# Kernel optimization log

Hardware: AMD Instinct MI355X
Metric: run time of the kernel (lower is better)

Reference implementation:

```python
import jax, jax.numpy as jnp
import numpy as np

TOPOLOGY = [-1, 0, 0, 0, 1, 2, 3, 4, 5, 6, 7, 8, 9, 9, 9, 12, 13, 14, 16, 17, 18, 19, 20, 21]
JOINT_WEIGHTS = np.ones(24, dtype=np.float32)
B1 = 1.0
B2 = 1.0


def quaternion_to_matrix(q):
    # pytorch3d convention: real part first (w, x, y, z)
    w, x, y, z = q[..., 0], q[..., 1], q[..., 2], q[..., 3]
    two_s = 2.0 / jnp.sum(q * q, axis=-1)
    o = jnp.stack([
        1 - two_s * (y * y + z * z), two_s * (x * y - z * w), two_s * (x * z + y * w),
        two_s * (x * y + z * w), 1 - two_s * (x * x + z * z), two_s * (y * z - x * w),
        two_s * (x * z - y * w), two_s * (y * z + x * w), 1 - two_s * (x * x + y * y),
    ], axis=-1)
    return o.reshape(q.shape[:-1] + (3, 3))


def fk(topology, X_m, X_t):
    # X_m: (bs, T, J*4+3), X_t: (bs, J, 3)
    J = len(topology)
    quat = X_m[..., :-3].reshape(X_m.shape[:-1] + (J, 4))
    local_rot = quaternion_to_matrix(quat)          # (bs, T, J, 3, 3)
    grots = [None] * J
    gtrs = [None] * J
    grots[0] = local_rot[..., 0, :, :]
    gtrs[0] = X_m[..., -3:]                          # root translation
    for i in range(1, J):
        pi = topology[i]
        grots[i] = jnp.matmul(grots[pi], local_rot[..., i, :, :])
        gtrs[i] = jnp.einsum('btij,bj->bti', grots[pi], X_t[:, i]) + gtrs[pi]
    return jnp.stack(grots, axis=-3), jnp.stack(gtrs, axis=-2)


def split_raw_motion(raw_motion):
    position = raw_motion[..., -3:]
    rotation = raw_motion[..., :-3]
    rotation = rotation.reshape(rotation.shape[:-1] + (-1, 4))
    norm = jnp.linalg.norm(rotation, axis=-1, keepdims=True)
    rotation = rotation / jnp.maximum(norm, 1e-12)
    return rotation, position


def weighted_mse(w, a, b):
    # w: (J,), a/b: (bs, T, J, C) -> per-joint weighted mean squared error
    return jnp.mean(w[None, None, :, None] * (a - b) ** 2)


def setup_inputs() -> dict:
    key = jax.random.key(0)
    k1, k2, k3, k4 = jax.random.split(key, 4)
    bs, T, J = 64, 2048, 24
    return {
        'Y_m': jax.random.normal(k1, (bs, T, J * 4 + 3), dtype=jnp.float32),
        'X_m': jax.random.normal(k2, (bs, T, J * 4 + 3), dtype=jnp.float32),
        'Y_t': jax.random.normal(k3, (bs, J, 3), dtype=jnp.float32),
        'X_t': jax.random.normal(k4, (bs, J, 3), dtype=jnp.float32),
    }


def reference(Y_m, X_m, Y_t, X_t):
    w = jnp.asarray(JOINT_WEIGHTS)
    rot_x, pos_x = split_raw_motion(X_m)
    rot_y, pos_y = split_raw_motion(Y_m)
    grot_y, gtr_y = fk(TOPOLOGY, Y_m, Y_t)
    grot_x, gtr_x = fk(TOPOLOGY, X_m, X_t)
    loss_rot = B1 * weighted_mse(w, rot_y, rot_x)
    loss_fk = B2 * (2.5 * weighted_mse(w, gtr_y, gtr_x)
                    + jnp.mean((pos_y - pos_x) ** 2))
    return loss_rot + loss_fk
```

## Files before the change

### kernel.cpp

```cpp
#include <hip/hip_runtime.h>

#define BS 64
#define TT 2048
#define NJ 24
#define ROWF 99
#define TROWS 128
#define BLOCK 128
#define NROWS (BS * TT)

__device__ __forceinline__ void quat2mat(float w, float x, float y, float z, float* R) {
  float s = 2.0f / (w*w + x*x + y*y + z*z);
  float xx = s*x*x, yy = s*y*y, zz = s*z*z;
  float xy = s*x*y, xz = s*x*z, yz = s*y*z;
  float xw = s*x*w, yw = s*y*w, zw = s*z*w;
  R[0] = 1.0f - (yy+zz); R[1] = xy - zw;        R[2] = xz + yw;
  R[3] = xy + zw;        R[4] = 1.0f - (xx+zz); R[5] = yz - xw;
  R[6] = xz - yw;        R[7] = yz + xw;        R[8] = 1.0f - (xx+yy);
}

__device__ __forceinline__ void mm3(const float* A, const float* B, float* C) {
#pragma unroll
  for (int r = 0; r < 3; ++r) {
#pragma unroll
    for (int c = 0; c < 3; ++c) {
      C[3*r+c] = fmaf(A[3*r], B[c], fmaf(A[3*r+1], B[3+c], A[3*r+2]*B[6+c]));
    }
  }
}

template<int PHASE>
__device__ __forceinline__ void fk_chain(const float* __restrict__ rowp,
                                         const float* __restrict__ tvec,
                                         float* __restrict__ gtr, float& gacc) {
  float G0[9], Ga[9], Gb[9], G9[9];
  float T0[3], Ta[3], Tb[3], T9[3];

  quat2mat(rowp[0], rowp[1], rowp[2], rowp[3], G0);
  T0[0] = rowp[96]; T0[1] = rowp[97]; T0[2] = rowp[98];
  if (PHASE == 0) { gtr[0] = T0[0]; gtr[1] = T0[1]; gtr[2] = T0[2]; }
  else { float d0 = T0[0]-gtr[0], d1 = T0[1]-gtr[1], d2 = T0[2]-gtr[2];
         gacc += d0*d0 + d1*d1 + d2*d2; }

#define STEP(c, Gp, Tp, Go, To) do { \
    float R[9]; quat2mat(rowp[4*(c)], rowp[4*(c)+1], rowp[4*(c)+2], rowp[4*(c)+3], R); \
    mm3(Gp, R, Go); \
    To[0] = fmaf(Gp[0], tvec[3*(c)], fmaf(Gp[1], tvec[3*(c)+1], fmaf(Gp[2], tvec[3*(c)+2], Tp[0]))); \
    To[1] = fmaf(Gp[3], tvec[3*(c)], fmaf(Gp[4], tvec[3*(c)+1], fmaf(Gp[5], tvec[3*(c)+2], Tp[1]))); \
    To[2] = fmaf(Gp[6], tvec[3*(c)], fmaf(Gp[7], tvec[3*(c)+1], fmaf(Gp[8], tvec[3*(c)+2], Tp[2]))); \
    if (PHASE == 0) { gtr[3*(c)] = To[0]; gtr[3*(c)+1] = To[1]; gtr[3*(c)+2] = To[2]; } \
    else { float d0 = To[0]-gtr[3*(c)], d1 = To[1]-gtr[3*(c)+1], d2 = To[2]-gtr[3*(c)+2]; \
           gacc += d0*d0 + d1*d1 + d2*d2; } \
  } while (0)

  STEP(1,  G0, T0, Ga, Ta); STEP(4,  Ga, Ta, Gb, Tb); STEP(7,  Gb, Tb, Ga, Ta); STEP(10, Ga, Ta, Gb, Tb);
  STEP(2,  G0, T0, Ga, Ta); STEP(5,  Ga, Ta, Gb, Tb); STEP(8,  Gb, Tb, Ga, Ta); STEP(11, Ga, Ta, Gb, Tb);
  STEP(3,  G0, T0, Ga, Ta); STEP(6,  Ga, Ta, Gb, Tb); STEP(9,  Gb, Tb, G9, T9);
  STEP(12, G9, T9, Ga, Ta); STEP(15, Ga, Ta, Gb, Tb);
  STEP(13, G9, T9, Ga, Ta); STEP(16, Ga, Ta, Gb, Tb); STEP(18, Gb, Tb, Ga, Ta); STEP(20, Ga, Ta, Gb, Tb); STEP(22, Gb, Tb, Ga, Ta);
  STEP(14, G9, T9, Ga, Ta); STEP(17, Ga, Ta, Gb, Tb); STEP(19, Gb, Tb, Ga, Ta); STEP(21, Ga, Ta, Gb, Tb); STEP(23, Gb, Tb, Ga, Ta);
#undef STEP
}

__global__ __launch_bounds__(BLOCK, 2) void motion_loss_kernel(
    const float* __restrict__ Ym, const float* __restrict__ Xm,
    const float* __restrict__ Yt, const float* __restrict__ Xt,
    float* __restrict__ out) {
  __shared__ __align__(16) float tile[TROWS * ROWF];
  __shared__ float tX[NJ * 3], tY[NJ * 3];

  const int tid = threadIdx.x;
  const int blk = blockIdx.x;
  const size_t row0 = (size_t)blk * TROWS;
  const int b = blk / (TT / TROWS);

  if (tid < NJ * 3) {
    tX[tid] = Xt[(size_t)b * NJ * 3 + tid];
    tY[tid] = Yt[(size_t)b * NJ * 3 + tid];
  }

  {
    const float4* g4 = (const float4*)(Xm + row0 * ROWF);
    float4* l4 = (float4*)tile;
    for (int k = tid; k < TROWS * ROWF / 4; k += BLOCK) l4[k] = g4[k];
  }
  __syncthreads();

  float gtrX[NJ * 3];
  float gacc = 0.0f, dummy = 0.0f;
  const float* rowp = tile + tid * ROWF;
  fk_chain<0>(rowp, tX, gtrX, dummy);
  __syncthreads();

  float rot_acc = 0.0f, pos_acc = 0.0f;
  const float* __restrict__ Yg = Ym + row0 * ROWF;
#pragma unroll 4
  for (int k = 0; k < NJ; ++k) {
    int q = tid + k * BLOCK;
    int r = q / NJ;
    int j = q - r * NJ;
    int off = r * ROWF + 4 * j;
    float y0 = Yg[off], y1 = Yg[off+1], y2 = Yg[off+2], y3 = Yg[off+3];
    float x0 = tile[off], x1 = tile[off+1], x2 = tile[off+2], x3 = tile[off+3];
    float ny = fmaxf(sqrtf(y0*y0 + y1*y1 + y2*y2 + y3*y3), 1e-12f);
    float nx = fmaxf(sqrtf(x0*x0 + x1*x1 + x2*x2 + x3*x3), 1e-12f);
    float iy = 1.0f / ny, ix = 1.0f / nx;
    float d0 = y0*iy - x0*ix, d1 = y1*iy - x1*ix;
    float d2 = y2*iy - x2*ix, d3 = y3*iy - x3*ix;
    rot_acc += d0*d0 + d1*d1 + d2*d2 + d3*d3;
    tile[off] = y0; tile[off+1] = y1; tile[off+2] = y2; tile[off+3] = y3;
  }
#pragma unroll
  for (int k = 0; k < 3; ++k) {
    int e = tid + k * BLOCK;
    int r = e / 3;
    int c = e - r * 3;
    int off = r * ROWF + 96 + c;
    float y = Yg[off], x = tile[off];
    float d = y - x;
    pos_acc += d * d;
    tile[off] = y;
  }
  __syncthreads();

  fk_chain<1>(rowp, tY, gtrX, gacc);

  const float c_rot = 1.0f / ((float)NROWS * NJ * 4);
  const float c_gtr = 2.5f / ((float)NROWS * NJ * 3);
  const float c_pos = 1.0f / ((float)NROWS * 3);
  float contrib = c_rot * rot_acc + c_gtr * gacc + c_pos * pos_acc;
#pragma unroll
  for (int o = 32; o > 0; o >>= 1) contrib += __shfl_down(contrib, o, 64);
  if ((tid & 63) == 0) atomicAdd(out, contrib);
}

extern "C" void kernel_launch(void* const* d_in, const int* in_sizes, int n_in,
                              void* d_out, int out_size, void* d_ws, size_t ws_size,
                              hipStream_t stream) {
  const float* Ym = (const float*)d_in[0];
  const float* Xm = (const float*)d_in[1];
  const float* Yt = (const float*)d_in[2];
  const float* Xt = (const float*)d_in[3];
  float* out = (float*)d_out;
  hipMemsetAsync(out, 0, sizeof(float), stream);
  motion_loss_kernel<<<NROWS / TROWS, BLOCK, 0, stream>>>(Ym, Xm, Yt, Xt, out);
}
```

Before: 167.9 us.

## Pair X and Y rows across adjacent lanes, exchange diffs via shuffles, drop LDS tiling

Each row is now handled by two adjacent threads, one running forward kinematics on X and the other on Y. Differences are exchanged with __shfl_xor instead of staging the X tile in LDS and keeping 72 per-thread registers of X translations. The joint tree is re-scheduled with four rotating register buffers, and leaf joints skip their unused matrix product. Global loads become uncoalesced strided unaligned float4 reads straight from memory, trading LDS staging for more parallelism and lower register pressure.

```diff
diff --git a/kernel.cpp b/kernel.cpp
--- a/kernel.cpp
+++ b/kernel.cpp
@@ -1,12 +1,15 @@
 #include <hip/hip_runtime.h>
 
+#define NJ 24
+#define ROWF 99
 #define BS 64
 #define TT 2048
-#define NJ 24
-#define ROWF 99
-#define TROWS 128
-#define BLOCK 128
 #define NROWS (BS * TT)
+#define BLOCK 256
+#define NTHREADS (2 * NROWS)
+
+typedef float f4_t __attribute__((ext_vector_type(4)));
+typedef f4_t float4u __attribute__((aligned(4)));
 
 __device__ __forceinline__ void quat2mat(float w, float x, float y, float z, float* R) {
   float s = 2.0f / (w*w + x*x + y*y + z*z);
@@ -20,117 +23,103 @@
 
 __device__ __forceinline__ void mm3(const float* A, const float* B, float* C) {
 #pragma unroll
-  for (int r = 0; r < 3; ++r) {
+  for (int r = 0; r < 3; ++r)
 #pragma unroll
-    for (int c = 0; c < 3; ++c) {
+    for (int c = 0; c < 3; ++c)
       C[3*r+c] = fmaf(A[3*r], B[c], fmaf(A[3*r+1], B[3+c], A[3*r+2]*B[6+c]));
-    }
-  }
 }
 
-template<int PHASE>
-__device__ __forceinline__ void fk_chain(const float* __restrict__ rowp,
-                                         const float* __restrict__ tvec,
-                                         float* __restrict__ gtr, float& gacc) {
-  float G0[9], Ga[9], Gb[9], G9[9];
-  float T0[3], Ta[3], Tb[3], T9[3];
+#define QMSE(q) ({ \
+  float _n  = sqrtf((q).x*(q).x + (q).y*(q).y + (q).z*(q).z + (q).w*(q).w); \
+  float _iv = 1.0f / fmaxf(_n, 1e-12f); \
+  float _a0 = (q).x*_iv, _a1 = (q).y*_iv, _a2 = (q).z*_iv, _a3 = (q).w*_iv; \
+  float _d0 = _a0 - __shfl_xor(_a0, 1, 64); \
+  float _d1 = _a1 - __shfl_xor(_a1, 1, 64); \
+  float _d2 = _a2 - __shfl_xor(_a2, 1, 64); \
+  float _d3 = _a3 - __shfl_xor(_a3, 1, 64); \
+  _d0*_d0 + _d1*_d1 + _d2*_d2 + _d3*_d3; })
 
-  quat2mat(rowp[0], rowp[1], rowp[2], rowp[3], G0);
-  T0[0] = rowp[96]; T0[1] = rowp[97]; T0[2] = rowp[98];
-  if (PHASE == 0) { gtr[0] = T0[0]; gtr[1] = T0[1]; gtr[2] = T0[2]; }
-  else { float d0 = T0[0]-gtr[0], d1 = T0[1]-gtr[1], d2 = T0[2]-gtr[2];
-         gacc += d0*d0 + d1*d1 + d2*d2; }
+#define TDIFF(t0, t1, t2) ({ \
+  float _e0 = (t0) - __shfl_xor((t0), 1, 64); \
+  float _e1 = (t1) - __shfl_xor((t1), 1, 64); \
+  float _e2 = (t2) - __shfl_xor((t2), 1, 64); \
+  _e0*_e0 + _e1*_e1 + _e2*_e2; })
 
-#define STEP(c, Gp, Tp, Go, To) do { \
-    float R[9]; quat2mat(rowp[4*(c)], rowp[4*(c)+1], rowp[4*(c)+2], rowp[4*(c)+3], R); \
-    mm3(Gp, R, Go); \
-    To[0] = fmaf(Gp[0], tvec[3*(c)], fmaf(Gp[1], tvec[3*(c)+1], fmaf(Gp[2], tvec[3*(c)+2], Tp[0]))); \
-    To[1] = fmaf(Gp[3], tvec[3*(c)], fmaf(Gp[4], tvec[3*(c)+1], fmaf(Gp[5], tvec[3*(c)+2], Tp[1]))); \
-    To[2] = fmaf(Gp[6], tvec[3*(c)], fmaf(Gp[7], tvec[3*(c)+1], fmaf(Gp[8], tvec[3*(c)+2], Tp[2]))); \
-    if (PHASE == 0) { gtr[3*(c)] = To[0]; gtr[3*(c)+1] = To[1]; gtr[3*(c)+2] = To[2]; } \
-    else { float d0 = To[0]-gtr[3*(c)], d1 = To[1]-gtr[3*(c)+1], d2 = To[2]-gtr[3*(c)+2]; \
-           gacc += d0*d0 + d1*d1 + d2*d2; } \
-  } while (0)
+#define STEP(c, GP, TP, GO, TO) do { \
+  float4u q = *(const float4u*)(rowp + 4*(c)); \
+  rot_acc += QMSE(q); \
+  float R[9]; quat2mat(q.x, q.y, q.z, q.w, R); \
+  mm3(GP, R, GO); \
+  float v0 = tv[3*(c)], v1 = tv[3*(c)+1], v2 = tv[3*(c)+2]; \
+  TO[0] = fmaf(GP[0], v0, fmaf(GP[1], v1, fmaf(GP[2], v2, TP[0]))); \
+  TO[1] = fmaf(GP[3], v0, fmaf(GP[4], v1, fmaf(GP[5], v2, TP[1]))); \
+  TO[2] = fmaf(GP[6], v0, fmaf(GP[7], v1, fmaf(GP[8], v2, TP[2]))); \
+  gacc += TDIFF(TO[0], TO[1], TO[2]); \
+} while (0)
 
-  STEP(1,  G0, T0, Ga, Ta); STEP(4,  Ga, Ta, Gb, Tb); STEP(7,  Gb, Tb, Ga, Ta); STEP(10, Ga, Ta, Gb, Tb);
-  STEP(2,  G0, T0, Ga, Ta); STEP(5,  Ga, Ta, Gb, Tb); STEP(8,  Gb, Tb, Ga, Ta); STEP(11, Ga, Ta, Gb, Tb);
-  STEP(3,  G0, T0, Ga, Ta); STEP(6,  Ga, Ta, Gb, Tb); STEP(9,  Gb, Tb, G9, T9);
-  STEP(12, G9, T9, Ga, Ta); STEP(15, Ga, Ta, Gb, Tb);
-  STEP(13, G9, T9, Ga, Ta); STEP(16, Ga, Ta, Gb, Tb); STEP(18, Gb, Tb, Ga, Ta); STEP(20, Ga, Ta, Gb, Tb); STEP(22, Gb, Tb, Ga, Ta);
-  STEP(14, G9, T9, Ga, Ta); STEP(17, Ga, Ta, Gb, Tb); STEP(19, Gb, Tb, Ga, Ta); STEP(21, Ga, Ta, Gb, Tb); STEP(23, Gb, Tb, Ga, Ta);
-#undef STEP
-}
+#define LEAF(c, GP, TP) do { \
+  float4u q = *(const float4u*)(rowp + 4*(c)); \
+  rot_acc += QMSE(q); \
+  float v0 = tv[3*(c)], v1 = tv[3*(c)+1], v2 = tv[3*(c)+2]; \
+  float t0 = fmaf(GP[0], v0, fmaf(GP[1], v1, fmaf(GP[2], v2, TP[0]))); \
+  float t1 = fmaf(GP[3], v0, fmaf(GP[4], v1, fmaf(GP[5], v2, TP[1]))); \
+  float t2 = fmaf(GP[6], v0, fmaf(GP[7], v1, fmaf(GP[8], v2, TP[2]))); \
+  gacc += TDIFF(t0, t1, t2); \
+} while (0)
 
-__global__ __launch_bounds__(BLOCK, 2) void motion_loss_kernel(
+__global__ __launch_bounds__(BLOCK, 4) void motion_loss_kernel(
     const float* __restrict__ Ym, const float* __restrict__ Xm,
     const float* __restrict__ Yt, const float* __restrict__ Xt,
     float* __restrict__ out) {
-  __shared__ __align__(16) float tile[TROWS * ROWF];
-  __shared__ float tX[NJ * 3], tY[NJ * 3];
+  const int gtid = blockIdx.x * BLOCK + threadIdx.x;
+  const int r   = gtid >> 1;
+  const int par = gtid & 1;
+  const float* __restrict__ rowp = (par ? Ym : Xm) + (size_t)r * ROWF;
+  const int b = r >> 11;
+  const float* __restrict__ tv = (par ? Yt : Xt) + (size_t)b * NJ * 3;
 
-  const int tid = threadIdx.x;
-  const int blk = blockIdx.x;
-  const size_t row0 = (size_t)blk * TROWS;
-  const int b = blk / (TT / TROWS);
+  float rot_acc = 0.0f, gacc = 0.0f;
+  float GA[9], GB[9], GC[9], GD[9];
+  float TA[3], TB[3], TC[3], TD[3];
 
-  if (tid < NJ * 3) {
-    tX[tid] = Xt[(size_t)b * NJ * 3 + tid];
-    tY[tid] = Yt[(size_t)b * NJ * 3 + tid];
-  }
+  float4u q0 = *(const float4u*)(rowp);
+  rot_acc += QMSE(q0);
+  quat2mat(q0.x, q0.y, q0.z, q0.w, GA);
+  TA[0] = rowp[96]; TA[1] = rowp[97]; TA[2] = rowp[98];
+  float rootd2 = TDIFF(TA[0], TA[1], TA[2]);
+  gacc += rootd2;
 
-  {
-    const float4* g4 = (const float4*)(Xm + row0 * ROWF);
-    float4* l4 = (float4*)tile;
-    for (int k = tid; k < TROWS * ROWF / 4; k += BLOCK) l4[k] = g4[k];
-  }
-  __syncthreads();
-
-  float gtrX[NJ * 3];
-  float gacc = 0.0f, dummy = 0.0f;
-  const float* rowp = tile + tid * ROWF;
-  fk_chain<0>(rowp, tX, gtrX, dummy);
-  __syncthreads();
-
-  float rot_acc = 0.0f, pos_acc = 0.0f;
-  const float* __restrict__ Yg = Ym + row0 * ROWF;
-#pragma unroll 4
-  for (int k = 0; k < NJ; ++k) {
-    int q = tid + k * BLOCK;
-    int r = q / NJ;
-    int j = q - r * NJ;
-    int off = r * ROWF + 4 * j;
-    float y0 = Yg[off], y1 = Yg[off+1], y2 = Yg[off+2], y3 = Yg[off+3];
-    float x0 = tile[off], x1 = tile[off+1], x2 = tile[off+2], x3 = tile[off+3];
-    float ny = fmaxf(sqrtf(y0*y0 + y1*y1 + y2*y2 + y3*y3), 1e-12f);
-    float nx = fmaxf(sqrtf(x0*x0 + x1*x1 + x2*x2 + x3*x3), 1e-12f);
-    float iy = 1.0f / ny, ix = 1.0f / nx;
-    float d0 = y0*iy - x0*ix, d1 = y1*iy - x1*ix;
-    float d2 = y2*iy - x2*ix, d3 = y3*iy - x3*ix;
-    rot_acc += d0*d0 + d1*d1 + d2*d2 + d3*d3;
-    tile[off] = y0; tile[off+1] = y1; tile[off+2] = y2; tile[off+3] = y3;
-  }
-#pragma unroll
-  for (int k = 0; k < 3; ++k) {
-    int e = tid + k * BLOCK;
-    int r = e / 3;
-    int c = e - r * 3;
-    int off = r * ROWF + 96 + c;
-    float y = Yg[off], x = tile[off];
-    float d = y - x;
-    pos_acc += d * d;
-    tile[off] = y;
-  }
-  __syncthreads();
-
-  fk_chain<1>(rowp, tY, gtrX, gacc);
+  STEP(1,  GA, TA, GB, TB);
+  STEP(2,  GA, TA, GC, TC);
+  STEP(3,  GA, TA, GD, TD);
+  STEP(4,  GB, TB, GA, TA);
+  STEP(5,  GC, TC, GB, TB);
+  STEP(6,  GD, TD, GC, TC);
+  STEP(7,  GA, TA, GD, TD);
+  STEP(8,  GB, TB, GA, TA);
+  STEP(9,  GC, TC, GB, TB);
+  LEAF(10, GD, TD);
+  LEAF(11, GA, TA);
+  STEP(12, GB, TB, GC, TC);
+  STEP(13, GB, TB, GD, TD);
+  STEP(14, GB, TB, GA, TA);
+  LEAF(15, GC, TC);
+  STEP(16, GD, TD, GB, TB);
+  STEP(17, GA, TA, GC, TC);
+  STEP(18, GB, TB, GD, TD);
+  STEP(19, GC, TC, GA, TA);
+  STEP(20, GD, TD, GB, TB);
+  STEP(21, GA, TA, GC, TC);
+  LEAF(22, GB, TB);
+  LEAF(23, GC, TC);
 
   const float c_rot = 1.0f / ((float)NROWS * NJ * 4);
   const float c_gtr = 2.5f / ((float)NROWS * NJ * 3);
   const float c_pos = 1.0f / ((float)NROWS * 3);
-  float contrib = c_rot * rot_acc + c_gtr * gacc + c_pos * pos_acc;
+  float contrib = 0.5f * (c_rot * rot_acc + c_gtr * gacc + c_pos * rootd2);
 #pragma unroll
   for (int o = 32; o > 0; o >>= 1) contrib += __shfl_down(contrib, o, 64);
-  if ((tid & 63) == 0) atomicAdd(out, contrib);
+  if ((threadIdx.x & 63) == 0) atomicAdd(out, contrib);
 }
 
 extern "C" void kernel_launch(void* const* d_in, const int* in_sizes, int n_in,
@@ -142,5 +131,5 @@
   const float* Xt = (const float*)d_in[3];
   float* out = (float*)d_out;
   hipMemsetAsync(out, 0, sizeof(float), stream);
-  motion_loss_kernel<<<NROWS / TROWS, BLOCK, 0, stream>>>(Ym, Xm, Yt, Xt, out);
+  motion_loss_kernel<<<NTHREADS / BLOCK, BLOCK, 0, stream>>>(Ym, Xm, Yt, Xt, out);
 }
```

Result: slower. 186.5 us (+11.1%).
